# Performance work log

Measured on AMD Instinct MI355X. Metric: run time of the kernel, lower is better.

The kernel has to match this reference:

```python
import jax, jax.numpy as jnp
import numpy as np
from jax import lax

B, h, Ch = 16, 8, 32
HW = 56
N = HW * HW
SPLITS = [64, 96, 96]  # [2*Ch, 3*Ch, 3*Ch] for windows {3,5,7}


def _dwconv(x, w, b, pad):
    # x: [B, C, H, W]; w: [C, 1, k, k] depthwise (feature_group_count=C)
    y = lax.conv_general_dilated(
        x, w, window_strides=(1, 1), padding=[(pad, pad), (pad, pad)],
        feature_group_count=x.shape[1],
        dimension_numbers=('NCHW', 'OIHW', 'NCHW'))
    return y + b[None, :, None, None]


def setup_inputs() -> dict:
    key = jax.random.key(0)
    ks = jax.random.split(key, 6)
    return {
        'q': jax.random.normal(ks[0], (B, h, N, Ch), dtype=jnp.float32),
        'v': jax.random.normal(ks[1], (B, h, N, Ch), dtype=jnp.float32),
        'w3': jax.random.normal(ks[2], (64, 1, 3, 3), dtype=jnp.float32) * 0.1,
        'b3': jnp.zeros((64,), dtype=jnp.float32),
        'w5': jax.random.normal(ks[3], (96, 1, 5, 5), dtype=jnp.float32) * 0.1,
        'b5': jnp.zeros((96,), dtype=jnp.float32),
        'w7': jax.random.normal(ks[4], (96, 1, 7, 7), dtype=jnp.float32) * 0.1,
        'b7': jnp.zeros((96,), dtype=jnp.float32),
        'H': HW,
        'W': HW,
    }


def reference(q, v, w3, b3, w5, b5, w7, b7, H, W):
    # q, v: [B, h, N, Ch]; N == H*W, Nv == N (same-resolution path, no interpolation)
    Bq, hh, Nq, C = q.shape
    # v: B h (H W) Ch -> B (h*Ch) H W
    v_img = jnp.transpose(v, (0, 1, 3, 2)).reshape(Bq, hh * C, H, W)
    v1, v2, v3 = jnp.split(v_img, np.cumsum(SPLITS)[:-1], axis=1)
    conv_v = jnp.concatenate([
        _dwconv(v1, w3, b3, 1),
        _dwconv(v2, w5, b5, 2),
        _dwconv(v3, w7, b7, 3),
    ], axis=1)  # [B, h*Ch, H, W]
    # B (h*Ch) H W -> B h (H W) Ch
    conv_v = conv_v.reshape(Bq, hh, C, H * W).transpose(0, 1, 3, 2)
    ev = q * conv_v  # [B, h, N, Ch]
    # transpose(1,2).flatten(2): [B, N, h*Ch]
    return jnp.transpose(ev, (0, 2, 1, 3)).reshape(Bq, Nq, hh * C)
```

## Files before the change

### kernel.cpp

```cpp
#include <hip/hip_runtime.h>
#include <cstddef>


#define BH 16
#define NH 8
#define CH 32
#define HW 56
#define NN (HW*HW)

typedef float f32x4 __attribute__((ext_vector_type(4)));
typedef unsigned int u32x4 __attribute__((ext_vector_type(4)));

__device__ __forceinline__ f32x4 bload(__amdgpu_buffer_rsrc_t rs, int voff) {
    u32x4 u = __builtin_amdgcn_raw_buffer_load_b128(rs, voff, 0, 0);
    f32x4 f;
    __builtin_memcpy(&f, &u, 16);
    return f;
}

template<int K>
__device__ __forceinline__ void run_head(
    const float* __restrict__ q, const float* __restrict__ v,
    const float* __restrict__ w, const float* __restrict__ bias,
    float* __restrict__ out, int b, int hh, int y0, int cbase,
    float* __restrict__ w_lds)
{
    constexpr int P = K / 2;
    constexpr int NR = 7 + K - 1;
    const int t = threadIdx.x;

    const int nw = K * K * CH;
    for (int i = t; i < nw; i += 256) {
        int tap = i >> 5, c = i & 31;
        w_lds[tap * CH + c] = w[(cbase + c) * (K * K) + tap];
    }
    __syncthreads();

    const int y    = y0 + (t >> 6);
    const int lane = t & 63;
    const int xseg = lane >> 3;
    const int chq  = lane & 7;
    const int x0   = xseg * 7;
    const int ch   = chq * 4;

    const size_t plane = ((size_t)b * NH + hh) * (size_t)NN * CH;
    const float* vb = v + plane;
    const float* qb = q + plane;

    int xoff[NR];
#pragma unroll
    for (int j = 0; j < NR; ++j)
        xoff[j] = ((x0 + j - P) * CH + ch) * 4;

    f32x4 bias4 = *(const f32x4*)(bias + cbase + ch);
    f32x4 acc[7];
#pragma unroll
    for (int i = 0; i < 7; ++i) acc[i] = bias4;

#pragma unroll
    for (int dy = 0; dy < K; ++dy) {
        const int yy = y + dy - P;
        const bool ok = (unsigned)yy < (unsigned)HW;
        const float* base = vb + (ptrdiff_t)yy * (HW * CH);
        __amdgpu_buffer_rsrc_t rs = __builtin_amdgcn_make_buffer_rsrc(
            (void*)base, (short)0, ok ? (HW * CH * 4) : 0, 0x00020000);

        f32x4 r[NR];
#pragma unroll
        for (int j = 0; j < NR; ++j) r[j] = bload(rs, xoff[j]);

#pragma unroll
        for (int dx = 0; dx < K; ++dx) {
            const f32x4 w4 = *(const f32x4*)(w_lds + (dy * K + dx) * CH + ch);
#pragma unroll
            for (int i = 0; i < 7; ++i)
                acc[i] += r[i + dx] * w4;
        }
    }

#pragma unroll
    for (int i = 0; i < 7; ++i) {
        const int n = y * HW + x0 + i;
        const f32x4 q4 = *(const f32x4*)(qb + (size_t)n * CH + ch);
        f32x4 o = acc[i] * q4;
        *(f32x4*)(out + ((size_t)b * NN + n) * (NH * CH) + hh * CH + ch) = o;
    }
}

__global__ __launch_bounds__(256, 4)
void clusterformer_fused(const float* __restrict__ q, const float* __restrict__ v,
                         const float* __restrict__ w3, const float* __restrict__ b3,
                         const float* __restrict__ w5, const float* __restrict__ b5,
                         const float* __restrict__ w7, const float* __restrict__ b7,
                         float* __restrict__ out)
{
    __shared__ float w_lds[49 * CH];

    const int bid  = blockIdx.x;
    const int p_lo = bid & 7;
    const int t2   = bid >> 3;
    const int p_hi = t2 / 14;
    const int yg   = t2 % 14;
    const int p    = p_hi * 8 + p_lo;
    const int b    = p & 15;
    const int hhp  = p >> 4;
    const int hh   = (hhp < 3) ? (5 + hhp) : ((hhp < 6) ? (hhp - 1) : (hhp - 6));
    const int y0   = yg * 4;

    if (hh < 2)      run_head<3>(q, v, w3, b3, out, b, hh, y0, hh * 32,       w_lds);
    else if (hh < 5) run_head<5>(q, v, w5, b5, out, b, hh, y0, hh * 32 - 64,  w_lds);
    else             run_head<7>(q, v, w7, b7, out, b, hh, y0, hh * 32 - 160, w_lds);
}

extern "C" void kernel_launch(void* const* d_in, const int* in_sizes, int n_in,
                              void* d_out, int out_size, void* d_ws, size_t ws_size,
                              hipStream_t stream) {
    const float* q  = (const float*)d_in[0];
    const float* v  = (const float*)d_in[1];
    const float* w3 = (const float*)d_in[2];
    const float* b3 = (const float*)d_in[3];
    const float* w5 = (const float*)d_in[4];
    const float* b5 = (const float*)d_in[5];
    const float* w7 = (const float*)d_in[6];
    const float* b7 = (const float*)d_in[7];
    float* out = (float*)d_out;

    const int grid = BH * NH * 14;
    clusterformer_fused<<<grid, 256, 0, stream>>>(q, v, w3, b3, w5, b5, w7, b7, out);
}
```

Measured before the change: 172.3 us.

## Stage input rows and outputs through per-wave LDS buffers for coalesced access

Each wave now loads every input row with fully contiguous 16-byte-per-lane global loads into a zero-padded LDS row buffer, then reads its strided halo windows from LDS rather than issuing overlapping strided global loads. Results are written back to LDS and re-read in a pixel-major order so the q loads and output stores become contiguous. This targets uncoalesced and redundant global traffic. The cost is extra LDS traffic and a larger LDS footprint, and the occupancy hint drops from 4 to 3 blocks. There is no barrier between the LDS writes and reads, which relies on each wave touching only its own buffer.

```diff
diff --git a/kernel.cpp b/kernel.cpp
--- a/kernel.cpp
+++ b/kernel.cpp
@@ -7,15 +7,16 @@
 #define CH 32
 #define HW 56
 #define NN (HW*HW)
+#define ROWB (HW*CH*4)
+#define BUF_PX 72
+#define BUF_FLOATS (BUF_PX*CH)
 
 typedef float f32x4 __attribute__((ext_vector_type(4)));
 typedef unsigned int u32x4 __attribute__((ext_vector_type(4)));
 
 __device__ __forceinline__ f32x4 bload(__amdgpu_buffer_rsrc_t rs, int voff) {
     u32x4 u = __builtin_amdgcn_raw_buffer_load_b128(rs, voff, 0, 0);
-    f32x4 f;
-    __builtin_memcpy(&f, &u, 16);
-    return f;
+    f32x4 f; __builtin_memcpy(&f, &u, 16); return f;
 }
 
 template<int K>
@@ -23,7 +24,7 @@
     const float* __restrict__ q, const float* __restrict__ v,
     const float* __restrict__ w, const float* __restrict__ bias,
     float* __restrict__ out, int b, int hh, int y0, int cbase,
-    float* __restrict__ w_lds)
+    float* __restrict__ w_lds, float* __restrict__ bufs)
 {
     constexpr int P = K / 2;
     constexpr int NR = 7 + K - 1;
@@ -36,21 +37,25 @@
     }
     __syncthreads();
 
-    const int y    = y0 + (t >> 6);
+    const int wid  = t >> 6;
     const int lane = t & 63;
+    float* wb = bufs + wid * BUF_FLOATS;
+
+    {
+        f32x4 z = {0.f, 0.f, 0.f, 0.f};
+        *(f32x4*)(wb + lane * 4) = z;
+        *(f32x4*)(wb + 64 * CH + lane * 4) = z;
+    }
+
+    const int y    = y0 + wid;
     const int xseg = lane >> 3;
     const int chq  = lane & 7;
     const int x0   = xseg * 7;
     const int ch   = chq * 4;
 
     const size_t plane = ((size_t)b * NH + hh) * (size_t)NN * CH;
-    const float* vb = v + plane;
-    const float* qb = q + plane;
-
-    int xoff[NR];
-#pragma unroll
-    for (int j = 0; j < NR; ++j)
-        xoff[j] = ((x0 + j - P) * CH + ch) * 4;
+    const float* vb   = v + plane;
+    const float* qrow = q + plane + (size_t)y * (HW * CH);
 
     f32x4 bias4 = *(const f32x4*)(bias + cbase + ch);
     f32x4 acc[7];
@@ -63,11 +68,20 @@
         const bool ok = (unsigned)yy < (unsigned)HW;
         const float* base = vb + (ptrdiff_t)yy * (HW * CH);
         __amdgpu_buffer_rsrc_t rs = __builtin_amdgcn_make_buffer_rsrc(
-            (void*)base, (short)0, ok ? (HW * CH * 4) : 0, 0x00020000);
+            (void*)base, (short)0, ok ? ROWB : 0, 0x00020000);
+
+        f32x4 ld[7];
+#pragma unroll
+        for (int k = 0; k < 7; ++k) ld[k] = bload(rs, k * 1024 + lane * 16);
+#pragma unroll
+        for (int k = 0; k < 7; ++k)
+            *(f32x4*)(wb + (k + 1) * 256 + lane * 4) = ld[k];
 
         f32x4 r[NR];
+        const float* rb = wb + (size_t)(x0 - P + 8) * CH + ch;
 #pragma unroll
-        for (int j = 0; j < NR; ++j) r[j] = bload(rs, xoff[j]);
+        for (int j = 0; j < NR; ++j)
+            r[j] = *(const f32x4*)(rb + j * CH);
 
 #pragma unroll
         for (int dx = 0; dx < K; ++dx) {
@@ -79,22 +93,30 @@
     }
 
 #pragma unroll
-    for (int i = 0; i < 7; ++i) {
-        const int n = y * HW + x0 + i;
-        const f32x4 q4 = *(const f32x4*)(qb + (size_t)n * CH + ch);
-        f32x4 o = acc[i] * q4;
-        *(f32x4*)(out + ((size_t)b * NN + n) * (NH * CH) + hh * CH + ch) = o;
+    for (int i = 0; i < 7; ++i)
+        *(f32x4*)(wb + (size_t)(x0 + i + 8) * CH + ch) = acc[i];
+
+    float* orow = out + ((size_t)b * NN + (size_t)y * HW) * (NH * CH) + hh * CH;
+    const int px_l = lane >> 3;
+    const int chl  = (lane & 7) * 4;
+#pragma unroll
+    for (int k = 0; k < 7; ++k) {
+        const f32x4 c4 = *(const f32x4*)(wb + (size_t)(k * 8 + px_l + 8) * CH + chl);
+        const f32x4 q4 = *(const f32x4*)(qrow + k * 256 + lane * 4);
+        const f32x4 o  = c4 * q4;
+        *(f32x4*)(orow + (size_t)(k * 8 + px_l) * (NH * CH) + chl) = o;
     }
 }
 
-__global__ __launch_bounds__(256, 4)
+__global__ __launch_bounds__(256, 3)
 void clusterformer_fused(const float* __restrict__ q, const float* __restrict__ v,
                          const float* __restrict__ w3, const float* __restrict__ b3,
                          const float* __restrict__ w5, const float* __restrict__ b5,
                          const float* __restrict__ w7, const float* __restrict__ b7,
                          float* __restrict__ out)
 {
-    __shared__ float w_lds[49 * CH];
+    __shared__ __align__(16) float bufs[4 * BUF_FLOATS];
+    __shared__ __align__(16) float w_lds[49 * CH];
 
     const int bid  = blockIdx.x;
     const int p_lo = bid & 7;
@@ -107,9 +129,9 @@
     const int hh   = (hhp < 3) ? (5 + hhp) : ((hhp < 6) ? (hhp - 1) : (hhp - 6));
     const int y0   = yg * 4;
 
-    if (hh < 2)      run_head<3>(q, v, w3, b3, out, b, hh, y0, hh * 32,       w_lds);
-    else if (hh < 5) run_head<5>(q, v, w5, b5, out, b, hh, y0, hh * 32 - 64,  w_lds);
-    else             run_head<7>(q, v, w7, b7, out, b, hh, y0, hh * 32 - 160, w_lds);
+    if (hh < 2)      run_head<3>(q, v, w3, b3, out, b, hh, y0, hh * 32,       w_lds, bufs);
+    else if (hh < 5) run_head<5>(q, v, w5, b5, out, b, hh, y0, hh * 32 - 64,  w_lds, bufs);
+    else             run_head<7>(q, v, w7, b7, out, b, hh, y0, hh * 32 - 160, w_lds, bufs);
 }
 
 extern "C" void kernel_launch(void* const* d_in, const int* in_sizes, int n_in,
```

Result: faster. 163.5 us (-5.1%).
